# Performance work log

Measured on AMD Instinct MI355X. Metric: run time of the kernel, lower is better.

Reference implementation:

```python
import jax, jax.numpy as jnp
import numpy as np

K_ORDER = 3
GRID_N = 10
GRID_LO, GRID_HI = -2.0, 2.0
LAYERS = [(49, 256), (256, 256), (256, 10)]
NCOEF = GRID_N + K_ORDER  # 13


def mish(x):
    return x * jnp.tanh(jax.nn.softplus(x))


def bspline_basis(x):
    # x: (B, in) -> basis (B, in, GRID_N + K_ORDER)
    h = (GRID_HI - GRID_LO) / GRID_N
    knots = GRID_LO + h * jnp.arange(-K_ORDER, GRID_N + K_ORDER + 1, dtype=x.dtype)  # (G+2k+1,)
    xx = x[..., None]
    B = ((xx >= knots[:-1]) & (xx < knots[1:])).astype(x.dtype)  # degree-0, (B,in,G+2k)
    for d in range(1, K_ORDER + 1):
        left = (xx - knots[: -(d + 1)]) / (knots[d:-1] - knots[: -(d + 1)]) * B[..., :-1]
        right = (knots[d + 1:] - xx) / (knots[d + 1:] - knots[1:-d]) * B[..., 1:]
        B = left + right
    return B  # (B, in, G+k)


def kan_layer(x, coef, scale_base, scale_sp, bias):
    # x: (B,in); coef: (in,out,G+k); scales: (in,out); bias: (out,)
    basis = bspline_basis(x)                                   # (B,in,G+k)
    spline = jnp.einsum('big,iog->bo', basis, coef * scale_sp[..., None])
    base = jnp.einsum('bi,io->bo', mish(x), scale_base)
    return base + spline + bias


def setup_inputs() -> dict:
    key = jax.random.key(0)
    ks = jax.random.split(key, 1 + 4 * len(LAYERS))
    inp = {'x': jax.random.normal(ks[0], (8192, 1, 28, 28), dtype=jnp.float32)}
    i = 1
    for li, (fin, fout) in enumerate(LAYERS, start=1):
        inp[f'coef{li}'] = 0.1 * jax.random.normal(ks[i], (fin, fout, NCOEF), dtype=jnp.float32); i += 1
        inp[f'sb{li}'] = 1.0 + 0.1 * jax.random.normal(ks[i], (fin, fout), dtype=jnp.float32); i += 1
        inp[f'sp{li}'] = 1.0 + 0.1 * jax.random.normal(ks[i], (fin, fout), dtype=jnp.float32); i += 1
        inp[f'b{li}'] = jnp.zeros((fout,), dtype=jnp.float32); i += 1
    return inp


def reference(x, coef1, sb1, sp1, b1, coef2, sb2, sp2, b2, coef3, sb3, sp3, b3):
    B = x.shape[0]
    # avg_pool2d(x, 4): 28x28 -> 7x7
    h = x.reshape(B, 1, 7, 4, 7, 4).mean(axis=(3, 5))
    h = h.reshape(B, 49)
    h = kan_layer(h, coef1, sb1, sp1, b1)
    h = kan_layer(h, coef2, sb2, sp2, b2)
    h = kan_layer(h, coef3, sb3, sp3, b3)
    return jax.nn.log_softmax(h, axis=1)
```

## Files before the change

### kernel.cpp

```cpp
#include <hip/hip_runtime.h>
#include <hip/hip_bf16.h>

typedef __bf16 bf16x8_t __attribute__((ext_vector_type(8)));
typedef float f32x4_t __attribute__((ext_vector_type(4)));
using bf16 = __hip_bfloat16;

__device__ __forceinline__ unsigned short f2bf_bits(float v) {
  __hip_bfloat16 h = __float2bfloat16(v);
  return *reinterpret_cast<unsigned short*>(&h);
}

__device__ __forceinline__ float mish_f(float x) {
  float z = __expf(x);
  float n = z * (z + 2.0f);
  float m = x * n / (n + 2.0f);
  return (x > 10.0f) ? x : m;
}

__device__ __forceinline__ void kan_feats28(bf16* dst, float x) {
  unsigned int* d32 = (unsigned int*)dst;
#pragma unroll
  for (int d = 0; d < 7; ++d) d32[d] = 0u;
  float t = (x + 3.2f) * 2.5f;
  if (t >= 0.0f && t < 16.0f) {
    float tf = floorf(t);
    int c = (int)tf;
    float u = t - tf;
    float um = 1.0f - u;
    float u2 = u * u, u3 = u2 * u;
    const float s6 = 1.0f / 6.0f;
    float w0 = um * um * um * s6;
    float w1 = (3.0f * u3 - 6.0f * u2 + 4.0f) * s6;
    float w2 = (-3.0f * u3 + 3.0f * u2 + 3.0f * u + 1.0f) * s6;
    float w3 = u3 * s6;
    int j0 = c - 3;
    if (j0 >= 0)               dst[j0]     = __float2bfloat16(w0);
    if (j0 >= -1 && j0 <= 11)  dst[j0 + 1] = __float2bfloat16(w1);
    if (j0 >= -2 && j0 <= 10)  dst[j0 + 2] = __float2bfloat16(w2);
    if (j0 <= 9)               dst[j0 + 3] = __float2bfloat16(w3);
  }
  dst[13] = __float2bfloat16(mish_f(x));
}

__global__ __launch_bounds__(256) void prep_all(
    const float* __restrict__ c1, const float* __restrict__ sb1, const float* __restrict__ sp1,
    const float* __restrict__ c2, const float* __restrict__ sb2, const float* __restrict__ sp2,
    const float* __restrict__ c3, const float* __restrict__ sb3, const float* __restrict__ sp3,
    bf16* __restrict__ W1f, bf16* __restrict__ W2f, bf16* __restrict__ W3f) {
  const int b = blockIdx.x, t = threadIdx.x;
  float vals[14];
  if (b < 49) {
    const int i = b, o = t;
    const int ntg = o >> 4, lrr = o & 15;
    const size_t io = (size_t)i * 256 + o;
    const float spv = sp1[io];
#pragma unroll
    for (int r = 0; r < 13; ++r) vals[r] = c1[io * 13 + r] * spv;
    vals[13] = sb1[io];
#pragma unroll
    for (int d = 0; d < 7; ++d) {
      const int k2 = i * 14 + 2 * d;
      const int s = k2 >> 5, r2 = k2 & 31;
      const size_t off = ((size_t)(s * 16 + ntg)) * 512 + lrr * 32 + (r2 >> 3) * 8 + (r2 & 7);
      *(unsigned int*)(W1f + off) = (unsigned int)f2bf_bits(vals[2 * d]) |
                                    ((unsigned int)f2bf_bits(vals[2 * d + 1]) << 16);
    }
  } else if (b == 49) {
    const int ntg = t >> 4, lrr = t & 15;
#pragma unroll
    for (int d = 0; d < 9; ++d) {
      const int k2 = 686 + 2 * d;
      const int r2 = k2 & 31;
      *(unsigned int*)(W1f + ((size_t)(21 * 16 + ntg)) * 512 + lrr * 32 + (r2 >> 3) * 8 + (r2 & 7)) = 0u;
    }
  } else if (b < 562) {
    if (t >= 128) return;
    const int idx = b - 50;
    const int i = idx >> 1;
    const int o = (idx & 1) * 128 + t;
    const int ntg = o >> 4, lrr = o & 15;
    const size_t io = (size_t)i * 256 + o;
    const float spv = sp2[io];
#pragma unroll
    for (int r = 0; r < 13; ++r) vals[r] = c2[io * 13 + r] * spv;
    vals[13] = sb2[io];
#pragma unroll
    for (int d = 0; d < 7; ++d) {
      const int k2 = i * 14 + 2 * d;
      const int s = k2 >> 5, r2 = k2 & 31;
      const size_t off = ((size_t)(s * 16 + ntg)) * 512 + lrr * 32 + (r2 >> 3) * 8 + (r2 & 7);
      *(unsigned int*)(W2f + off) = (unsigned int)f2bf_bits(vals[2 * d]) |
                                    ((unsigned int)f2bf_bits(vals[2 * d + 1]) << 16);
    }
  } else {
    const int i = b - 562, o = t;
    if (o < 10) {
      const size_t io = (size_t)i * 10 + o;
      const float spv = sp3[io];
#pragma unroll
      for (int r = 0; r < 13; ++r) vals[r] = c3[io * 13 + r] * spv;
      vals[13] = sb3[io];
#pragma unroll
      for (int d = 0; d < 7; ++d) {
        const int k2 = i * 14 + 2 * d;
        const int s = k2 >> 5, r2 = k2 & 31;
        const size_t off = (size_t)s * 512 + o * 32 + (r2 >> 3) * 8 + (r2 & 7);
        *(unsigned int*)(W3f + off) = (unsigned int)f2bf_bits(vals[2 * d]) |
                                      ((unsigned int)f2bf_bits(vals[2 * d + 1]) << 16);
      }
    } else if (o < 16) {
#pragma unroll
      for (int d = 0; d < 7; ++d) {
        const int k2 = i * 14 + 2 * d;
        const int s = k2 >> 5, r2 = k2 & 31;
        *(unsigned int*)(W3f + (size_t)s * 512 + o * 32 + (r2 >> 3) * 8 + (r2 & 7)) = 0u;
      }
    }
  }
}

__global__ __launch_bounds__(1024, 4) void meganet(
    const float* __restrict__ x, const bf16* __restrict__ W1f,
    const bf16* __restrict__ W2f, const bf16* __restrict__ W3f,
    const float* __restrict__ b1, const float* __restrict__ b2,
    const float* __restrict__ b3, float* __restrict__ out) {
  __shared__ __align__(16) char lds[73728];
  float* const Hs = (float*)lds;
  bf16* const Ach0 = (bf16*)(lds + 36864);
  bf16* const Ach1 = (bf16*)(lds + 51712);
  float* const P = (float*)(lds + 66560);
  float* const xs = (float*)lds;
  float* const Red = (float*)(lds + 36864);
  float* const V = (float*)(lds + 51712);

  const int t = threadIdx.x;
  const int w = t >> 6, lane = t & 63, quad = lane >> 4, lr = lane & 15;
  const int tr = t >> 5 >= 16 ? (t >> 4) & 31 : (t >> 4) & 31, ej = t & 15;
  const int r0 = blockIdx.x * 32;
  const int foff = lr * 32 + quad * 8;

  for (int h = 0; h < 2; ++h) {
    const float4* src = (const float4*)x + (size_t)(r0 + h * 16) * 196;
    float4* xd = (float4*)xs;
#pragma unroll
    for (int l = 0; l < 4; ++l) {
      const int idx = t + l * 1024;
      if (idx < 3136) xd[idx] = src[idx];
    }
    __syncthreads();
    if (t < 784) {
      const int img = t / 49, p = t - img * 49;
      const int oh = p / 7, ow = p - oh * 7;
      const float* xi = xs + img * 784 + oh * 112 + ow * 4;
      float s = 0.f;
#pragma unroll
      for (int rr = 0; rr < 4; ++rr)
#pragma unroll
        for (int cc = 0; cc < 4; ++cc) s += xi[rr * 28 + cc];
      P[(h * 16 + img) * 56 + p] = s * (1.0f / 16.0f);
    }
    __syncthreads();
  }

  f32x4_t acc1[2];
  acc1[0] = (f32x4_t){0.f, 0.f, 0.f, 0.f};
  acc1[1] = acc1[0];
  bf16x8_t q[12];
#pragma unroll
  for (int s = 0; s < 12; ++s)
    q[s] = *(const bf16x8_t*)(W1f + (size_t)(s * 16 + w) * 512 + foff);
  if (t >= 512) kan_feats28(Ach0 + tr * 232 + ej * 14, P[tr * 56 + ej]);
  __syncthreads();
#pragma unroll
  for (int c = 0; c < 4; ++c) {
    const bf16* const Ac = (c & 1) ? Ach1 : Ach0;
    bf16* const An = (c & 1) ? Ach0 : Ach1;
    const int nks = (c < 3) ? 7 : 1;
#pragma unroll
    for (int ks = 0; ks < 7; ++ks) {
      if (ks >= nks) continue;
      const int kk = c * 7 + ks;
      const int sl = kk % 12;
      bf16x8_t bb = q[sl];
      if (kk + 12 < 22)
        q[sl] = *(const bf16x8_t*)(W1f + (size_t)((kk + 12) * 16 + w) * 512 + foff);
#pragma unroll
      for (int m = 0; m < 2; ++m) {
        bf16x8_t a = *(const bf16x8_t*)(Ac + (m * 16 + lr) * 232 + ks * 32 + quad * 8);
        acc1[m] = __builtin_amdgcn_mfma_f32_16x16x32_bf16(a, bb, acc1[m], 0, 0, 0);
      }
    }
    const bool doF = ((c & 1) == 0) ? (t < 512) : (t >= 512);
    if (doF) {
      if (c < 2) {
        kan_feats28(An + tr * 232 + ej * 14, P[tr * 56 + (c + 1) * 16 + ej]);
      } else if (c == 2) {
        if (ej == 0) kan_feats28(An + tr * 232, P[tr * 56 + 48]);
        else if (ej == 1) {
          unsigned int* z = (unsigned int*)(An + tr * 232 + 14);
#pragma unroll
          for (int d = 0; d < 9; ++d) z[d] = 0u;
        }
      }
    }
    __syncthreads();
  }
  {
    const int col = w * 16 + lr;
    const float bn = b1[col];
#pragma unroll
    for (int m = 0; m < 2; ++m) {
      f32x4_t v;
#pragma unroll
      for (int r = 0; r < 4; ++r) v[r] = acc1[m][r] + bn;
      *(f32x4_t*)(Hs + col * 36 + m * 16 + quad * 4) = v;
    }
  }
  __syncthreads();

  f32x4_t acc2[2];
  acc2[0] = (f32x4_t){0.f, 0.f, 0.f, 0.f};
  acc2[1] = acc2[0];
#pragma unroll
  for (int s = 0; s < 12; ++s)
    q[s] = *(const bf16x8_t*)(W2f + (size_t)(s * 16 + w) * 512 + foff);
  if (t >= 512) kan_feats28(Ach0 + tr * 232 + ej * 14, Hs[ej * 36 + tr]);
  __syncthreads();
#pragma unroll
  for (int c = 0; c < 16; ++c) {
    const bf16* const Ac = (c & 1) ? Ach1 : Ach0;
    bf16* const An = (c & 1) ? Ach0 : Ach1;
#pragma unroll
    for (int ks = 0; ks < 7; ++ks) {
      const int kk = c * 7 + ks;
      const int sl = kk % 12;
      bf16x8_t bb = q[sl];
      if (kk + 12 < 112)
        q[sl] = *(const bf16x8_t*)(W2f + (size_t)((kk + 12) * 16 + w) * 512 + foff);
#pragma unroll
      for (int m = 0; m < 2; ++m) {
        bf16x8_t a = *(const bf16x8_t*)(Ac + (m * 16 + lr) * 232 + ks * 32 + quad * 8);
        acc2[m] = __builtin_amdgcn_mfma_f32_16x16x32_bf16(a, bb, acc2[m], 0, 0, 0);
      }
    }
    const bool doF = ((c & 1) == 0) ? (t < 512) : (t >= 512);
    if (doF && c < 15)
      kan_feats28(An + tr * 232 + ej * 14, Hs[((c + 1) * 16 + ej) * 36 + tr]);
    __syncthreads();
  }
  {
    const int col = w * 16 + lr;
    const float bn = b2[col];
#pragma unroll
    for (int m = 0; m < 2; ++m) {
      f32x4_t v;
#pragma unroll
      for (int r = 0; r < 4; ++r) v[r] = acc2[m][r] + bn;
      *(f32x4_t*)(Hs + col * 36 + m * 16 + quad * 4) = v;
    }
  }
  __syncthreads();

  f32x4_t acc3 = {0.f, 0.f, 0.f, 0.f};
  const int mh = w / 7, ks3 = w % 7;
  bf16x8_t q3[4];
  if (w < 14) {
#pragma unroll
    for (int s = 0; s < 4; ++s)
      q3[s] = *(const bf16x8_t*)(W3f + (size_t)(s * 7 + ks3) * 512 + foff);
  }
  if (t < 512) kan_feats28(Ach0 + tr * 232 + ej * 14, Hs[ej * 36 + tr]);
  __syncthreads();
#pragma unroll
  for (int c = 0; c < 16; ++c) {
    const bf16* const Ac = (c & 1) ? Ach1 : Ach0;
    bf16* const An = (c & 1) ? Ach0 : Ach1;
    if (w < 14) {
      bf16x8_t bb = q3[c & 3];
      if (c + 4 < 16)
        q3[c & 3] = *(const bf16x8_t*)(W3f + (size_t)((c + 4) * 7 + ks3) * 512 + foff);
      bf16x8_t a = *(const bf16x8_t*)(Ac + (mh * 16 + lr) * 232 + ks3 * 32 + quad * 8);
      acc3 = __builtin_amdgcn_mfma_f32_16x16x32_bf16(a, bb, acc3, 0, 0, 0);
    }
    const bool doF = ((c & 1) == 0) ? (t >= 512) : (t < 512);
    if (doF && c < 15)
      kan_feats28(An + tr * 232 + ej * 14, Hs[((c + 1) * 16 + ej) * 36 + tr]);
    __syncthreads();
  }
  if (w < 14) {
#pragma unroll
    for (int r = 0; r < 4; ++r)
      Red[w * 256 + (quad * 4 + r) * 16 + lr] = acc3[r];
  }
  __syncthreads();
  if (t < 512) {
    float s = (ej < 10) ? b3[ej] : 0.f;
    const int mh2 = tr >> 4, lrow = tr & 15;
#pragma unroll
    for (int ks = 0; ks < 7; ++ks) s += Red[(mh2 * 7 + ks) * 256 + lrow * 16 + ej];
    V[tr * 16 + ej] = s;
  }
  __syncthreads();
  if (t < 32) {
    float vv[10];
#pragma unroll
    for (int o = 0; o < 10; ++o) vv[o] = V[t * 16 + o];
    float mx = vv[0];
#pragma unroll
    for (int o = 1; o < 10; ++o) mx = fmaxf(mx, vv[o]);
    float se = 0.f;
#pragma unroll
    for (int o = 0; o < 10; ++o) se += expf(vv[o] - mx);
    const float l = mx + logf(se);
#pragma unroll
    for (int o = 0; o < 10; ++o) out[(size_t)(r0 + t) * 10 + o] = vv[o] - l;
  }
}

extern "C" void kernel_launch(void* const* d_in, const int* in_sizes, int n_in,
                              void* d_out, int out_size, void* d_ws, size_t ws_size,
                              hipStream_t stream) {
  const float* x = (const float*)d_in[0];
  const float* coef1 = (const float*)d_in[1];
  const float* sb1 = (const float*)d_in[2];
  const float* sp1 = (const float*)d_in[3];
  const float* b1 = (const float*)d_in[4];
  const float* coef2 = (const float*)d_in[5];
  const float* sb2 = (const float*)d_in[6];
  const float* sp2 = (const float*)d_in[7];
  const float* b2 = (const float*)d_in[8];
  const float* coef3 = (const float*)d_in[9];
  const float* sb3 = (const float*)d_in[10];
  const float* sp3 = (const float*)d_in[11];
  const float* b3 = (const float*)d_in[12];
  float* out = (float*)d_out;

  char* ws = (char*)d_ws;
  bf16* W1f = (bf16*)ws;
  bf16* W2f = (bf16*)(ws + 360448);
  bf16* W3f = (bf16*)(ws + 2195456);

  prep_all<<<818, 256, 0, stream>>>(coef1, sb1, sp1, coef2, sb2, sp2,
                                    coef3, sb3, sp3, W1f, W2f, W3f);
  meganet<<<256, 1024, 0, stream>>>(x, W1f, W2f, W3f, b1, b2, b3, out);
}
```

Baseline: 141.7 us.

## Specialize warps into MFMA consumers and feature producers per layer

Splits the 16 waves into 8 compute waves, each owning two 16-column output tiles with a 4-deep weight prefetch ring, and 8 producer waves that build B-spline features for the next chunk. Previously all 16 waves did MFMA and features were split by halves. Layer 3 now uses 7 waves handling both row halves instead of 14. The aim is to overlap feature generation with matrix work and to reuse each A fragment across two B tiles. In exchange, per-wave MFMA work doubles and the weight prefetch depth drops.

```diff
diff --git a/kernel.cpp b/kernel.cpp
--- a/kernel.cpp
+++ b/kernel.cpp
@@ -135,9 +135,11 @@
 
   const int t = threadIdx.x;
   const int w = t >> 6, lane = t & 63, quad = lane >> 4, lr = lane & 15;
-  const int tr = t >> 5 >= 16 ? (t >> 4) & 31 : (t >> 4) & 31, ej = t & 15;
+  const int tr = (t >> 4) & 31, ej = t & 15;
   const int r0 = blockIdx.x * 32;
   const int foff = lr * 32 + quad * 8;
+  const bool cons = (w < 8);
+  const int ntg0 = 2 * w;
 
   for (int h = 0; h < 2; ++h) {
     const float4* src = (const float4*)x + (size_t)(r0 + h * 16) * 196;
@@ -162,36 +164,47 @@
     __syncthreads();
   }
 
-  f32x4_t acc1[2];
-  acc1[0] = (f32x4_t){0.f, 0.f, 0.f, 0.f};
-  acc1[1] = acc1[0];
-  bf16x8_t q[12];
-#pragma unroll
-  for (int s = 0; s < 12; ++s)
-    q[s] = *(const bf16x8_t*)(W1f + (size_t)(s * 16 + w) * 512 + foff);
-  if (t >= 512) kan_feats28(Ach0 + tr * 232 + ej * 14, P[tr * 56 + ej]);
+  f32x4_t acc[2][2];
+#pragma unroll
+  for (int m = 0; m < 2; ++m)
+#pragma unroll
+    for (int n = 0; n < 2; ++n) acc[m][n] = (f32x4_t){0.f, 0.f, 0.f, 0.f};
+
+  bf16x8_t q0[4], q1[4];
+  if (cons) {
+#pragma unroll
+    for (int s = 0; s < 4; ++s) {
+      q0[s] = *(const bf16x8_t*)(W1f + (size_t)(s * 16 + ntg0) * 512 + foff);
+      q1[s] = *(const bf16x8_t*)(W1f + (size_t)(s * 16 + ntg0 + 1) * 512 + foff);
+    }
+  } else {
+    kan_feats28(Ach0 + tr * 232 + ej * 14, P[tr * 56 + ej]);
+  }
   __syncthreads();
 #pragma unroll
   for (int c = 0; c < 4; ++c) {
     const bf16* const Ac = (c & 1) ? Ach1 : Ach0;
     bf16* const An = (c & 1) ? Ach0 : Ach1;
-    const int nks = (c < 3) ? 7 : 1;
-#pragma unroll
-    for (int ks = 0; ks < 7; ++ks) {
-      if (ks >= nks) continue;
-      const int kk = c * 7 + ks;
-      const int sl = kk % 12;
-      bf16x8_t bb = q[sl];
-      if (kk + 12 < 22)
-        q[sl] = *(const bf16x8_t*)(W1f + (size_t)((kk + 12) * 16 + w) * 512 + foff);
-#pragma unroll
-      for (int m = 0; m < 2; ++m) {
-        bf16x8_t a = *(const bf16x8_t*)(Ac + (m * 16 + lr) * 232 + ks * 32 + quad * 8);
-        acc1[m] = __builtin_amdgcn_mfma_f32_16x16x32_bf16(a, bb, acc1[m], 0, 0, 0);
-      }
-    }
-    const bool doF = ((c & 1) == 0) ? (t < 512) : (t >= 512);
-    if (doF) {
+    if (cons) {
+      const int nks = (c < 3) ? 7 : 1;
+#pragma unroll
+      for (int ks = 0; ks < 7; ++ks) {
+        if (ks >= nks) continue;
+        const int kk = c * 7 + ks;
+        const int sl = kk & 3;
+        bf16x8_t bb0 = q0[sl], bb1 = q1[sl];
+        if (kk + 4 < 22) {
+          q0[sl] = *(const bf16x8_t*)(W1f + (size_t)((kk + 4) * 16 + ntg0) * 512 + foff);
+          q1[sl] = *(const bf16x8_t*)(W1f + (size_t)((kk + 4) * 16 + ntg0 + 1) * 512 + foff);
+        }
+#pragma unroll
+        for (int m = 0; m < 2; ++m) {
+          bf16x8_t a = *(const bf16x8_t*)(Ac + (m * 16 + lr) * 232 + ks * 32 + quad * 8);
+          acc[m][0] = __builtin_amdgcn_mfma_f32_16x16x32_bf16(a, bb0, acc[m][0], 0, 0, 0);
+          acc[m][1] = __builtin_amdgcn_mfma_f32_16x16x32_bf16(a, bb1, acc[m][1], 0, 0, 0);
+        }
+      }
+    } else {
       if (c < 2) {
         kan_feats28(An + tr * 232 + ej * 14, P[tr * 56 + (c + 1) * 16 + ej]);
       } else if (c == 2) {
@@ -205,99 +218,118 @@
     }
     __syncthreads();
   }
-  {
-    const int col = w * 16 + lr;
-    const float bn = b1[col];
-#pragma unroll
-    for (int m = 0; m < 2; ++m) {
-      f32x4_t v;
-#pragma unroll
-      for (int r = 0; r < 4; ++r) v[r] = acc1[m][r] + bn;
-      *(f32x4_t*)(Hs + col * 36 + m * 16 + quad * 4) = v;
-    }
-  }
-  __syncthreads();
-
-  f32x4_t acc2[2];
-  acc2[0] = (f32x4_t){0.f, 0.f, 0.f, 0.f};
-  acc2[1] = acc2[0];
-#pragma unroll
-  for (int s = 0; s < 12; ++s)
-    q[s] = *(const bf16x8_t*)(W2f + (size_t)(s * 16 + w) * 512 + foff);
-  if (t >= 512) kan_feats28(Ach0 + tr * 232 + ej * 14, Hs[ej * 36 + tr]);
+  if (cons) {
+#pragma unroll
+    for (int m = 0; m < 2; ++m)
+#pragma unroll
+      for (int n = 0; n < 2; ++n) {
+        const int col = w * 32 + n * 16 + lr;
+        const float bn = b1[col];
+        f32x4_t v;
+#pragma unroll
+        for (int r = 0; r < 4; ++r) v[r] = acc[m][n][r] + bn;
+        *(f32x4_t*)(Hs + col * 36 + m * 16 + quad * 4) = v;
+      }
+  }
+  __syncthreads();
+
+#pragma unroll
+  for (int m = 0; m < 2; ++m)
+#pragma unroll
+    for (int n = 0; n < 2; ++n) acc[m][n] = (f32x4_t){0.f, 0.f, 0.f, 0.f};
+  if (cons) {
+#pragma unroll
+    for (int s = 0; s < 4; ++s) {
+      q0[s] = *(const bf16x8_t*)(W2f + (size_t)(s * 16 + ntg0) * 512 + foff);
+      q1[s] = *(const bf16x8_t*)(W2f + (size_t)(s * 16 + ntg0 + 1) * 512 + foff);
+    }
+  } else {
+    kan_feats28(Ach0 + tr * 232 + ej * 14, Hs[ej * 36 + tr]);
+  }
   __syncthreads();
 #pragma unroll
   for (int c = 0; c < 16; ++c) {
     const bf16* const Ac = (c & 1) ? Ach1 : Ach0;
     bf16* const An = (c & 1) ? Ach0 : Ach1;
-#pragma unroll
-    for (int ks = 0; ks < 7; ++ks) {
-      const int kk = c * 7 + ks;
-      const int sl = kk % 12;
-      bf16x8_t bb = q[sl];
-      if (kk + 12 < 112)
-        q[sl] = *(const bf16x8_t*)(W2f + (size_t)((kk + 12) * 16 + w) * 512 + foff);
-#pragma unroll
-      for (int m = 0; m < 2; ++m) {
-        bf16x8_t a = *(const bf16x8_t*)(Ac + (m * 16 + lr) * 232 + ks * 32 + quad * 8);
-        acc2[m] = __builtin_amdgcn_mfma_f32_16x16x32_bf16(a, bb, acc2[m], 0, 0, 0);
-      }
-    }
-    const bool doF = ((c & 1) == 0) ? (t < 512) : (t >= 512);
-    if (doF && c < 15)
+    if (cons) {
+#pragma unroll
+      for (int ks = 0; ks < 7; ++ks) {
+        const int kk = c * 7 + ks;
+        const int sl = kk & 3;
+        bf16x8_t bb0 = q0[sl], bb1 = q1[sl];
+        if (kk + 4 < 112) {
+          q0[sl] = *(const bf16x8_t*)(W2f + (size_t)((kk + 4) * 16 + ntg0) * 512 + foff);
+          q1[sl] = *(const bf16x8_t*)(W2f + (size_t)((kk + 4) * 16 + ntg0 + 1) * 512 + foff);
+        }
+#pragma unroll
+        for (int m = 0; m < 2; ++m) {
+          bf16x8_t a = *(const bf16x8_t*)(Ac + (m * 16 + lr) * 232 + ks * 32 + quad * 8);
+          acc[m][0] = __builtin_amdgcn_mfma_f32_16x16x32_bf16(a, bb0, acc[m][0], 0, 0, 0);
+          acc[m][1] = __builtin_amdgcn_mfma_f32_16x16x32_bf16(a, bb1, acc[m][1], 0, 0, 0);
+        }
+      }
+    } else if (c < 15) {
       kan_feats28(An + tr * 232 + ej * 14, Hs[((c + 1) * 16 + ej) * 36 + tr]);
-    __syncthreads();
-  }
-  {
-    const int col = w * 16 + lr;
-    const float bn = b2[col];
-#pragma unroll
-    for (int m = 0; m < 2; ++m) {
-      f32x4_t v;
-#pragma unroll
-      for (int r = 0; r < 4; ++r) v[r] = acc2[m][r] + bn;
-      *(f32x4_t*)(Hs + col * 36 + m * 16 + quad * 4) = v;
-    }
-  }
-  __syncthreads();
-
-  f32x4_t acc3 = {0.f, 0.f, 0.f, 0.f};
-  const int mh = w / 7, ks3 = w % 7;
+    }
+    __syncthreads();
+  }
+  if (cons) {
+#pragma unroll
+    for (int m = 0; m < 2; ++m)
+#pragma unroll
+      for (int n = 0; n < 2; ++n) {
+        const int col = w * 32 + n * 16 + lr;
+        const float bn = b2[col];
+        f32x4_t v;
+#pragma unroll
+        for (int r = 0; r < 4; ++r) v[r] = acc[m][n][r] + bn;
+        *(f32x4_t*)(Hs + col * 36 + m * 16 + quad * 4) = v;
+      }
+  }
+  __syncthreads();
+
+  f32x4_t acc3[2];
+  acc3[0] = (f32x4_t){0.f, 0.f, 0.f, 0.f};
+  acc3[1] = acc3[0];
   bf16x8_t q3[4];
-  if (w < 14) {
+  if (w < 7) {
 #pragma unroll
     for (int s = 0; s < 4; ++s)
-      q3[s] = *(const bf16x8_t*)(W3f + (size_t)(s * 7 + ks3) * 512 + foff);
-  }
-  if (t < 512) kan_feats28(Ach0 + tr * 232 + ej * 14, Hs[ej * 36 + tr]);
+      q3[s] = *(const bf16x8_t*)(W3f + (size_t)(s * 7 + w) * 512 + foff);
+  } else if (!cons) {
+    kan_feats28(Ach0 + tr * 232 + ej * 14, Hs[ej * 36 + tr]);
+  }
   __syncthreads();
 #pragma unroll
   for (int c = 0; c < 16; ++c) {
     const bf16* const Ac = (c & 1) ? Ach1 : Ach0;
     bf16* const An = (c & 1) ? Ach0 : Ach1;
-    if (w < 14) {
+    if (w < 7) {
       bf16x8_t bb = q3[c & 3];
       if (c + 4 < 16)
-        q3[c & 3] = *(const bf16x8_t*)(W3f + (size_t)((c + 4) * 7 + ks3) * 512 + foff);
-      bf16x8_t a = *(const bf16x8_t*)(Ac + (mh * 16 + lr) * 232 + ks3 * 32 + quad * 8);
-      acc3 = __builtin_amdgcn_mfma_f32_16x16x32_bf16(a, bb, acc3, 0, 0, 0);
-    }
-    const bool doF = ((c & 1) == 0) ? (t >= 512) : (t < 512);
-    if (doF && c < 15)
+        q3[c & 3] = *(const bf16x8_t*)(W3f + (size_t)((c + 4) * 7 + w) * 512 + foff);
+#pragma unroll
+      for (int m = 0; m < 2; ++m) {
+        bf16x8_t a = *(const bf16x8_t*)(Ac + (m * 16 + lr) * 232 + w * 32 + quad * 8);
+        acc3[m] = __builtin_amdgcn_mfma_f32_16x16x32_bf16(a, bb, acc3[m], 0, 0, 0);
+      }
+    } else if (!cons && c < 15) {
       kan_feats28(An + tr * 232 + ej * 14, Hs[((c + 1) * 16 + ej) * 36 + tr]);
-    __syncthreads();
-  }
-  if (w < 14) {
-#pragma unroll
-    for (int r = 0; r < 4; ++r)
-      Red[w * 256 + (quad * 4 + r) * 16 + lr] = acc3[r];
+    }
+    __syncthreads();
+  }
+  if (w < 7) {
+#pragma unroll
+    for (int m = 0; m < 2; ++m)
+#pragma unroll
+      for (int r = 0; r < 4; ++r)
+        Red[w * 512 + (m * 16 + quad * 4 + r) * 16 + lr] = acc3[m][r];
   }
   __syncthreads();
   if (t < 512) {
     float s = (ej < 10) ? b3[ej] : 0.f;
-    const int mh2 = tr >> 4, lrow = tr & 15;
-#pragma unroll
-    for (int ks = 0; ks < 7; ++ks) s += Red[(mh2 * 7 + ks) * 256 + lrow * 16 + ej];
+#pragma unroll
+    for (int ks = 0; ks < 7; ++ks) s += Red[ks * 512 + tr * 16 + ej];
     V[tr * 16 + ej] = s;
   }
   __syncthreads();
```

Result: no change. 139.0 us (median of 2 runs) (-1.9%).
